# Performance work log

Hardware: AMD Instinct MI355X
Metric: run time of the kernel (lower is better)

## Reference

```python
import jax, jax.numpy as jnp
import numpy as np

AREA = 4
HEADS = 8

def conv1x1(x, W, b):
    # x: [B,C,H,W], W: [O,C], b: [O]
    return jnp.einsum('bchw,oc->bohw', x, W) + b[None, :, None, None]

def dwconv5(x, W, b):
    # depthwise 5x5, pad 2, groups = C; W: [C,1,5,5]
    C = x.shape[1]
    y = jax.lax.conv_general_dilated(
        x, W, window_strides=(1, 1), padding=[(2, 2), (2, 2)],
        dimension_numbers=('NCHW', 'OIHW', 'NCHW'), feature_group_count=C)
    return y + b[None, :, None, None]

def setup_inputs() -> dict:
    key = jax.random.key(0)
    ks = jax.random.split(key, 9)
    B, C, H, W = 4, 256, 64, 64
    s = 0.05
    return {
        'x': jax.random.normal(ks[0], (B, C, H, W), jnp.float32),
        'Wqk': jax.random.normal(ks[1], (2 * C, C), jnp.float32) * s,
        'bqk': jax.random.normal(ks[2], (2 * C,), jnp.float32) * s,
        'Wv': jax.random.normal(ks[3], (C, C), jnp.float32) * s,
        'bv': jax.random.normal(ks[4], (C,), jnp.float32) * s,
        'Wpe': jax.random.normal(ks[5], (C, 1, 5, 5), jnp.float32) * s,
        'bpe': jax.random.normal(ks[6], (C,), jnp.float32) * s,
        'Wproj': jax.random.normal(ks[7], (C, C), jnp.float32) * s,
        'bproj': jax.random.normal(ks[8], (C,), jnp.float32) * s,
    }

def reference(x, Wqk, bqk, Wv, bv, Wpe, bpe, Wproj, bproj):
    B, C, H, W = x.shape
    N = H * W
    hd = C // HEADS
    # qk / v projections (1x1 conv + folded BN bias, no activation)
    qk = conv1x1(x, Wqk, bqk).reshape(B, 2 * C, N).transpose(0, 2, 1)  # [B,N,2C]
    v4 = conv1x1(x, Wv, bv)                                            # [B,C,H,W]
    pp = dwconv5(v4, Wpe, bpe)                                         # positional enc
    v = v4.reshape(B, C, N).transpose(0, 2, 1)                         # [B,N,C]
    # area split: [B*area, N/area, .]
    Ba, Na = B * AREA, N // AREA
    qk = qk.reshape(Ba, Na, 2 * C)
    v = v.reshape(Ba, Na, C)
    q, k = qk[..., :C], qk[..., C:]
    q = q.reshape(Ba, Na, HEADS, hd)
    k = k.reshape(Ba, Na, HEADS, hd)
    v = v.reshape(Ba, Na, HEADS, hd)
    # manual softmax attention: (q^T k) * d^-0.5 -> softmax -> weight v
    attn = jnp.einsum('bqhd,bkhd->bhqk', q, k) * (hd ** -0.5)
    attn = jax.nn.softmax(attn, axis=-1)
    out = jnp.einsum('bhqk,bkhd->bqhd', attn, v)                       # [Ba,Na,H,hd]
    # merge areas back and go to NCHW
    out = out.reshape(B, N, C).reshape(B, H, W, C).transpose(0, 3, 1, 2)
    return conv1x1(out + pp, Wproj, bproj)
```

## Files before the change

kernel.cpp:

```cpp
#include <hip/hip_runtime.h>

typedef unsigned short u16;
typedef unsigned int u32;
using f32x4  = __attribute__((ext_vector_type(4))) float;
using u32x2  = __attribute__((ext_vector_type(2))) u32;
using u32x4  = __attribute__((ext_vector_type(4))) u32;
using bf16x8 = __attribute__((ext_vector_type(8))) short;

__device__ __forceinline__ u16 f2b(float f) {
  union { float f; u32 u; } v; v.f = f;
  return (u16)((v.u + 0x7FFFu + ((v.u >> 16) & 1u)) >> 16);
}
__device__ __forceinline__ float b2f(u16 u) {
  union { u32 u; float f; } v; v.u = ((u32)u) << 16;
  return v.f;
}
__device__ __forceinline__ u32 pk2(float a, float b) {
  u32 r;
  asm("v_cvt_pk_bf16_f32 %0, %1, %2" : "=v"(r) : "v"(a), "v"(b));
  return r;
}

__global__ __launch_bounds__(256) void kconvert(
    const float* __restrict__ Wqk, const float* __restrict__ Wv,
    const float* __restrict__ Wproj, u16* __restrict__ dst) {
  int e = (blockIdx.x * 256 + threadIdx.x) * 4;
  f32x4 v;
  if (e < 131072)      v = *(const f32x4*)(Wqk + e);
  else if (e < 196608) v = *(const f32x4*)(Wv + (e - 131072));
  else                 v = *(const f32x4*)(Wproj + (e - 196608));
  u32* d = (u32*)(dst + e);
  d[0] = (u32)f2b(v[0]) | ((u32)f2b(v[1]) << 16);
  d[1] = (u32)f2b(v[2]) | ((u32)f2b(v[3]) << 16);
}

__global__ __launch_bounds__(512) void kqkv(
    const float* __restrict__ x,
    const u16* __restrict__ Wqk_bf, const float* __restrict__ bqk,
    const u16* __restrict__ Wv_bf,  const float* __restrict__ bv,
    u16* __restrict__ qk_tm, u16* __restrict__ v_cm) {
  __shared__ __align__(16) u16 xs[64 * 264];
  const int bid = blockIdx.x;
  const int b   = bid >> 6;
  const int n0  = (bid & 63) * 64;
  const int tid = threadIdx.x;

  {
    const int part = tid & 15, cr = tid >> 4;
    #pragma unroll
    for (int p = 0; p < 8; ++p) {
      const int c = p * 32 + cr;
      f32x4 v = *(const f32x4*)(x + (size_t)(b * 256 + c) * 4096 + n0 + part * 4);
      const int t0 = part * 4;
      xs[(t0 + 0) * 264 + c] = f2b(v[0]);
      xs[(t0 + 1) * 264 + c] = f2b(v[1]);
      xs[(t0 + 2) * 264 + c] = f2b(v[2]);
      xs[(t0 + 3) * 264 + c] = f2b(v[3]);
    }
  }
  __syncthreads();

  const int wave = tid >> 6, l = tid & 63, lg = l & 15, lq = l >> 4;

  for (int ot = wave; ot < 48; ot += 8) {
    if (ot < 32) {
      bf16x8 bfr[8];
      const u16* wrow = Wqk_bf + (ot * 16 + lg) * 256 + lq * 8;
      #pragma unroll
      for (int kk = 0; kk < 8; ++kk) bfr[kk] = *(const bf16x8*)(wrow + kk * 32);
      const float bias = bqk[ot * 16 + lg];
      #pragma unroll
      for (int ts = 0; ts < 4; ++ts) {
        f32x4 acc = {0.f, 0.f, 0.f, 0.f};
        #pragma unroll
        for (int kk = 0; kk < 8; ++kk) {
          bf16x8 af = *(const bf16x8*)(&xs[(ts * 16 + lg) * 264 + kk * 32 + lq * 8]);
          acc = __builtin_amdgcn_mfma_f32_16x16x32_bf16(af, bfr[kk], acc, 0, 0, 0);
        }
        u16* dst = qk_tm + (size_t)(b * 4096 + n0 + ts * 16 + lq * 4) * 512 + ot * 16 + lg;
        #pragma unroll
        for (int r = 0; r < 4; ++r) dst[(size_t)r * 512] = f2b(acc[r] + bias);
      }
    } else {
      const int o2 = ot - 32;
      bf16x8 afw[8];
      const u16* wrow = Wv_bf + (o2 * 16 + lg) * 256 + lq * 8;
      #pragma unroll
      for (int kk = 0; kk < 8; ++kk) afw[kk] = *(const bf16x8*)(wrow + kk * 32);
      float bvr[4];
      #pragma unroll
      for (int r = 0; r < 4; ++r) bvr[r] = bv[o2 * 16 + lq * 4 + r];
      #pragma unroll
      for (int ts = 0; ts < 4; ++ts) {
        f32x4 acc = {0.f, 0.f, 0.f, 0.f};
        #pragma unroll
        for (int kk = 0; kk < 8; ++kk) {
          bf16x8 bfx = *(const bf16x8*)(&xs[(ts * 16 + lg) * 264 + kk * 32 + lq * 8]);
          acc = __builtin_amdgcn_mfma_f32_16x16x32_bf16(afw[kk], bfx, acc, 0, 0, 0);
        }
        #pragma unroll
        for (int r = 0; r < 4; ++r) {
          const int o = o2 * 16 + lq * 4 + r;
          v_cm[(size_t)(b * 256 + o) * 4096 + n0 + ts * 16 + lg] = f2b(acc[r] + bvr[r]);
        }
      }
    }
  }
}

__global__ __launch_bounds__(256) void kdw(
    const u16* __restrict__ v_cm, const float* __restrict__ Wpe,
    const float* __restrict__ bpe, u16* __restrict__ pp) {
  __shared__ __align__(16) u16 vsh[5 * 64 * 64];
  __shared__ float wsh[64 * 25];
  const int bid = blockIdx.x;
  const int ct = bid & 3, h = (bid >> 2) & 63, b = bid >> 8;
  const int c0 = ct * 64;
  const int tid = threadIdx.x;

  for (int i = tid; i < 64 * 25; i += 256) wsh[i] = Wpe[(c0 + i / 25) * 25 + i % 25];
  #pragma unroll
  for (int uu = 0; uu < 10; ++uu) {
    const int u = uu * 256 + tid;
    const int dy = u >> 9, rem = u & 511, c = rem >> 3, part = rem & 7;
    const int hy = h + dy - 2;
    u32x4 val = {0, 0, 0, 0};
    if (hy >= 0 && hy < 64)
      val = *(const u32x4*)(v_cm + (size_t)(b * 256 + c0 + c) * 4096 + hy * 64 + part * 8);
    *(u32x4*)(&vsh[(dy * 64 + c) * 64 + part * 8]) = val;
  }
  __syncthreads();

  const int c = tid >> 2, w0 = (tid & 3) * 16;
  float acc16[16];
  const float bias = bpe[c0 + c];
  #pragma unroll
  for (int i = 0; i < 16; ++i) acc16[i] = bias;
  const float* wc = &wsh[c * 25];
  #pragma unroll
  for (int dy = 0; dy < 5; ++dy) {
    const u16* row = &vsh[(dy * 64 + c) * 64];
    float rowv[20];
    #pragma unroll
    for (int j = 0; j < 20; ++j) {
      const int ww = w0 + j - 2;
      rowv[j] = (ww >= 0 && ww < 64) ? b2f(row[ww]) : 0.f;
    }
    #pragma unroll
    for (int dx = 0; dx < 5; ++dx) {
      const float wv = wc[dy * 5 + dx];
      #pragma unroll
      for (int wi = 0; wi < 16; ++wi) acc16[wi] += rowv[wi + dx] * wv;
    }
  }
  u32x4 o0, o1;
  #pragma unroll
  for (int i = 0; i < 4; ++i)
    o0[i] = (u32)f2b(acc16[2 * i]) | ((u32)f2b(acc16[2 * i + 1]) << 16);
  #pragma unroll
  for (int i = 0; i < 4; ++i)
    o1[i] = (u32)f2b(acc16[8 + 2 * i]) | ((u32)f2b(acc16[9 + 2 * i]) << 16);
  u16* dst = pp + (size_t)(b * 256 + c0 + c) * 4096 + h * 64 + w0;
  *(u32x4*)(dst) = o0;
  *(u32x4*)(dst + 8) = o1;
}

__global__ __launch_bounds__(256) void kattn(
    const u16* __restrict__ qk_tm, const u16* __restrict__ v_cm,
    u16* __restrict__ out_tm) {
  __shared__ __align__(16) char pbuf[4][32 * 128];

  const int bid = blockIdx.x;
  const int xcd = bid & 7, idx = bid >> 3;
  const int pair = xcd * 16 + (idx >> 3);
  const int qb = idx & 7;
  const int h = pair & 7, ba = pair >> 3;
  const int b = ba >> 2, area = ba & 3;
  const size_t row_base = (size_t)b * 4096 + area * 1024;

  const int tid = threadIdx.x;
  const int wave = tid >> 6, l = tid & 63, lg = l & 15, lq = l >> 4;
  char* pbc = pbuf[wave];
  const int swz = (lg & 7) << 4;
  const float kscale = 0.25503484f;

  bf16x8 bQ[2];
  #pragma unroll
  for (int s = 0; s < 2; ++s) {
    const size_t qrow = row_base + qb * 128 + wave * 32 + s * 16 + lg;
    bQ[s] = *(const bf16x8*)(qk_tm + qrow * 512 + h * 32 + lq * 8);
  }

  const u16* Kbase = qk_tm + row_base * 512 + 256 + h * 32 + lq * 8;
  const u16* Vbase = v_cm + (size_t)(b * 256 + h * 32) * 4096 + area * 1024 + lq * 8;

  f32x4 accO[2][2];
  float dAcc[2] = {0.f, 0.f};
  #pragma unroll
  for (int s = 0; s < 2; ++s)
    #pragma unroll
    for (int d = 0; d < 2; ++d) accO[s][d] = (f32x4){0.f, 0.f, 0.f, 0.f};

  bf16x8 fK0[4], fV0[4], fK1[4], fV1[4];

  auto LOAD = [&](bf16x8* fK, bf16x8* fV, int kb) {
    #pragma unroll
    for (int t = 0; t < 4; ++t)
      fK[t] = *(const bf16x8*)(Kbase + (size_t)(kb * 64 + t * 16 + lg) * 512);
    #pragma unroll
    for (int kk = 0; kk < 2; ++kk)
      #pragma unroll
      for (int dt = 0; dt < 2; ++dt)
        fV[kk * 2 + dt] = *(const bf16x8*)(Vbase + (size_t)(dt * 16 + lg) * 4096 + kb * 64 + kk * 32);
  };

  auto COMP = [&](bf16x8* fK, bf16x8* fV) {
    f32x4 sc[2][4];
    #pragma unroll
    for (int s = 0; s < 2; ++s)
      #pragma unroll
      for (int t = 0; t < 4; ++t) {
        f32x4 z = {0.f, 0.f, 0.f, 0.f};
        sc[s][t] = __builtin_amdgcn_mfma_f32_16x16x32_bf16(fK[t], bQ[s], z, 0, 0, 0);
      }
    #pragma unroll
    for (int s = 0; s < 2; ++s)
      #pragma unroll
      for (int t = 0; t < 4; ++t) {
        const float e0 = __builtin_amdgcn_exp2f(sc[s][t][0] * kscale);
        const float e1 = __builtin_amdgcn_exp2f(sc[s][t][1] * kscale);
        const float e2 = __builtin_amdgcn_exp2f(sc[s][t][2] * kscale);
        const float e3 = __builtin_amdgcn_exp2f(sc[s][t][3] * kscale);
        dAcc[s] += (e0 + e1) + (e2 + e3);
        u32x2 w = {pk2(e0, e1), pk2(e2, e3)};
        *(u32x2*)(pbc + (s * 16 + lg) * 128 + ((t * 32 + lq * 8) ^ swz)) = w;
      }
    asm volatile("s_waitcnt lgkmcnt(0)" ::: "memory");
    __builtin_amdgcn_sched_barrier(0);
    #pragma unroll
    for (int s = 0; s < 2; ++s)
      #pragma unroll
      for (int kk = 0; kk < 2; ++kk) {
        bf16x8 aP = *(const bf16x8*)(pbc + (s * 16 + lg) * 128 + ((kk * 64 + lq * 16) ^ swz));
        #pragma unroll
        for (int dt = 0; dt < 2; ++dt)
          accO[s][dt] = __builtin_amdgcn_mfma_f32_16x16x32_bf16(aP, fV[kk * 2 + dt], accO[s][dt], 0, 0, 0);
      }
  };

  LOAD(fK0, fV0, 0);
  for (int kb = 0; kb < 16; kb += 2) {
    LOAD(fK1, fV1, kb + 1);
    COMP(fK0, fV0);
    if (kb + 2 < 16) LOAD(fK0, fV0, kb + 2);
    COMP(fK1, fV1);
  }

  #pragma unroll
  for (int s = 0; s < 2; ++s) {
    float d = dAcc[s];
    d += __shfl_xor(d, 16);
    d += __shfl_xor(d, 32);
    #pragma unroll
    for (int r = 0; r < 4; ++r) {
      const float den = __shfl(d, lq * 4 + r);
      const float inv = __builtin_amdgcn_rcpf(den);
      const size_t row = row_base + qb * 128 + wave * 32 + s * 16 + lq * 4 + r;
      u16* dst = out_tm + row * 256 + h * 32 + lg;
      dst[0]  = f2b(accO[s][0][r] * inv);
      dst[16] = f2b(accO[s][1][r] * inv);
    }
  }
}

__global__ __launch_bounds__(512) void kproj(
    const u16* __restrict__ out_tm, const u16* __restrict__ pp,
    const u16* __restrict__ Wproj_bf, const float* __restrict__ bproj,
    float* __restrict__ out) {
  __shared__ __align__(16) u16 as_[64 * 264];
  const int bid = blockIdx.x;
  const int b = bid >> 6;
  const int n0 = (bid & 63) * 64;
  const int tid = threadIdx.x;
  {
    const int r = tid >> 3, qp = tid & 7;
    const u32x4* src = (const u32x4*)(out_tm + (size_t)(b * 4096 + n0 + r) * 256 + qp * 32);
    #pragma unroll
    for (int j = 0; j < 4; ++j)
      *(u32x4*)(&as_[r * 264 + qp * 32 + j * 8]) = src[j];
  }
  __syncthreads();
  {
    const int part = tid & 7;
    #pragma unroll
    for (int pass = 0; pass < 4; ++pass) {
      const int c = pass * 64 + (tid >> 3);
      u32x4 v = *(const u32x4*)(pp + (size_t)(b * 256 + c) * 4096 + n0 + part * 8);
      #pragma unroll
      for (int jj = 0; jj < 4; ++jj) {
        u32 w = v[jj];
        u16* q0 = &as_[(part * 8 + jj * 2) * 264 + c];
        *q0 = f2b(b2f(*q0) + b2f((u16)(w & 0xffffu)));
        u16* q1 = &as_[(part * 8 + jj * 2 + 1) * 264 + c];
        *q1 = f2b(b2f(*q1) + b2f((u16)(w >> 16)));
      }
    }
  }
  __syncthreads();
  const int wave = tid >> 6, l = tid & 63, lg = l & 15, lq = l >> 4;
  #pragma unroll
  for (int oi = 0; oi < 2; ++oi) {
    const int ot = oi * 8 + wave;
    bf16x8 afw[8];
    const u16* wrow = Wproj_bf + (ot * 16 + lg) * 256 + lq * 8;
    #pragma unroll
    for (int kk = 0; kk < 8; ++kk) afw[kk] = *(const bf16x8*)(wrow + kk * 32);
    float bpr[4];
    #pragma unroll
    for (int r = 0; r < 4; ++r) bpr[r] = bproj[ot * 16 + lq * 4 + r];
    #pragma unroll
    for (int ts = 0; ts < 4; ++ts) {
      f32x4 acc = {0.f, 0.f, 0.f, 0.f};
      #pragma unroll
      for (int kk = 0; kk < 8; ++kk) {
        bf16x8 bfx = *(const bf16x8*)(&as_[(ts * 16 + lg) * 264 + kk * 32 + lq * 8]);
        acc = __builtin_amdgcn_mfma_f32_16x16x32_bf16(afw[kk], bfx, acc, 0, 0, 0);
      }
      #pragma unroll
      for (int r = 0; r < 4; ++r) {
        const int o = ot * 16 + lq * 4 + r;
        out[(size_t)(b * 256 + o) * 4096 + n0 + ts * 16 + lg] = acc[r] + bpr[r];
      }
    }
  }
}

extern "C" void kernel_launch(void* const* d_in, const int* in_sizes, int n_in,
                              void* d_out, int out_size, void* d_ws, size_t ws_size,
                              hipStream_t stream) {
  const float* x     = (const float*)d_in[0];
  const float* Wqk   = (const float*)d_in[1];
  const float* bqk   = (const float*)d_in[2];
  const float* Wv    = (const float*)d_in[3];
  const float* bv    = (const float*)d_in[4];
  const float* Wpe   = (const float*)d_in[5];
  const float* bpe   = (const float*)d_in[6];
  const float* Wproj = (const float*)d_in[7];
  const float* bproj = (const float*)d_in[8];
  float* out = (float*)d_out;

  char* ws = (char*)d_ws;
  u16* qk_tm  = (u16*)(ws);
  u16* v_cm   = (u16*)(ws + 16777216);
  u16* pp     = (u16*)(ws + 25165824);
  u16* out_tm = (u16*)(ws + 33554432);
  u16* wbf    = (u16*)(ws + 41943040);
  u16* Wqk_bf = wbf;
  u16* Wv_bf = wbf + 131072;
  u16* Wproj_bf = wbf + 196608;

  kconvert<<<256, 256, 0, stream>>>(Wqk, Wv, Wproj, wbf);
  kqkv<<<256, 512, 0, stream>>>(x, Wqk_bf, bqk, Wv_bf, bv, qk_tm, v_cm);
  kdw<<<1024, 256, 0, stream>>>(v_cm, Wpe, bpe, pp);
  kattn<<<1024, 256, 0, stream>>>(qk_tm, v_cm, out_tm);
  kproj<<<256, 512, 0, stream>>>(out_tm, pp, Wproj_bf, bproj, out);
}
```

Measured before the change: 123.4 us.

## Split attention key range across wave pairs and reduce partials in LDS

Each attention block now covers 64 query rows instead of 128. Pairs of waves split the 1024-key range in half, and each wave loops over 8 key blocks instead of 16. The second wave of each pair writes its partial output accumulators and row sums to LDS, and the first wave adds them before normalizing and storing. This doubles the grid to 2048 blocks and halves the serial loop length per wave, which adds parallelism and shortens the tail. The cost is reloading Q tiles across more blocks, two extra block barriers and an LDS round trip for the reduction. It is only correct without a running max because the softmax uses plain exp sums.

```diff
diff --git a/kernel.cpp b/kernel.cpp
--- a/kernel.cpp
+++ b/kernel.cpp
@@ -169,17 +169,19 @@
     const u16* __restrict__ qk_tm, const u16* __restrict__ v_cm,
     u16* __restrict__ out_tm) {
   __shared__ __align__(16) char pbuf[4][32 * 128];
+  __shared__ float dbuf[4][32];
 
   const int bid = blockIdx.x;
   const int xcd = bid & 7, idx = bid >> 3;
-  const int pair = xcd * 16 + (idx >> 3);
-  const int qb = idx & 7;
+  const int pair = xcd * 16 + (idx >> 4);
+  const int qb = idx & 15;
   const int h = pair & 7, ba = pair >> 3;
   const int b = ba >> 2, area = ba & 3;
   const size_t row_base = (size_t)b * 4096 + area * 1024;
 
   const int tid = threadIdx.x;
   const int wave = tid >> 6, l = tid & 63, lg = l & 15, lq = l >> 4;
+  const int qhalf = wave >> 1, khalf = wave & 1;
   char* pbc = pbuf[wave];
   const int swz = (lg & 7) << 4;
   const float kscale = 0.25503484f;
@@ -187,12 +189,12 @@
   bf16x8 bQ[2];
   #pragma unroll
   for (int s = 0; s < 2; ++s) {
-    const size_t qrow = row_base + qb * 128 + wave * 32 + s * 16 + lg;
+    const size_t qrow = row_base + qb * 64 + qhalf * 32 + s * 16 + lg;
     bQ[s] = *(const bf16x8*)(qk_tm + qrow * 512 + h * 32 + lq * 8);
   }
 
-  const u16* Kbase = qk_tm + row_base * 512 + 256 + h * 32 + lq * 8;
-  const u16* Vbase = v_cm + (size_t)(b * 256 + h * 32) * 4096 + area * 1024 + lq * 8;
+  const u16* Kbase = qk_tm + (row_base + khalf * 512) * 512 + 256 + h * 32 + lq * 8;
+  const u16* Vbase = v_cm + (size_t)(b * 256 + h * 32) * 4096 + area * 1024 + khalf * 512 + lq * 8;
 
   f32x4 accO[2][2];
   float dAcc[2] = {0.f, 0.f};
@@ -249,26 +251,59 @@
   };
 
   LOAD(fK0, fV0, 0);
-  for (int kb = 0; kb < 16; kb += 2) {
+  for (int kb = 0; kb < 8; kb += 2) {
     LOAD(fK1, fV1, kb + 1);
     COMP(fK0, fV0);
-    if (kb + 2 < 16) LOAD(fK0, fV0, kb + 2);
+    if (kb + 2 < 8) LOAD(fK0, fV0, kb + 2);
     COMP(fK1, fV1);
   }
 
+  float dred[2];
   #pragma unroll
   for (int s = 0; s < 2; ++s) {
     float d = dAcc[s];
     d += __shfl_xor(d, 16);
     d += __shfl_xor(d, 32);
-    #pragma unroll
-    for (int r = 0; r < 4; ++r) {
-      const float den = __shfl(d, lq * 4 + r);
-      const float inv = __builtin_amdgcn_rcpf(den);
-      const size_t row = row_base + qb * 128 + wave * 32 + s * 16 + lq * 4 + r;
-      u16* dst = out_tm + row * 256 + h * 32 + lg;
-      dst[0]  = f2b(accO[s][0][r] * inv);
-      dst[16] = f2b(accO[s][1][r] * inv);
+    dred[s] = d;
+  }
+
+  __syncthreads();
+  if (khalf == 1) {
+    float* cb = (float*)pbuf[wave];
+    #pragma unroll
+    for (int s = 0; s < 2; ++s)
+      #pragma unroll
+      for (int dt = 0; dt < 2; ++dt)
+        #pragma unroll
+        for (int r = 0; r < 4; ++r)
+          cb[((s * 2 + dt) * 4 + r) * 64 + lq * 16 + lg] = accO[s][dt][r];
+    if (lq == 0) {
+      dbuf[wave][lg]      = dred[0];
+      dbuf[wave][16 + lg] = dred[1];
+    }
+  }
+  __syncthreads();
+  if (khalf == 0) {
+    const float* cb = (const float*)pbuf[wave + 1];
+    #pragma unroll
+    for (int s = 0; s < 2; ++s)
+      #pragma unroll
+      for (int dt = 0; dt < 2; ++dt)
+        #pragma unroll
+        for (int r = 0; r < 4; ++r)
+          accO[s][dt][r] += cb[((s * 2 + dt) * 4 + r) * 64 + lq * 16 + lg];
+    #pragma unroll
+    for (int s = 0; s < 2; ++s) {
+      const float dfull = dred[s] + dbuf[wave + 1][s * 16 + lg];
+      #pragma unroll
+      for (int r = 0; r < 4; ++r) {
+        const float den = __shfl(dfull, lq * 4 + r);
+        const float inv = __builtin_amdgcn_rcpf(den);
+        const size_t row = row_base + qb * 64 + qhalf * 32 + s * 16 + lq * 4 + r;
+        u16* dst = out_tm + row * 256 + h * 32 + lg;
+        dst[0]  = f2b(accO[s][0][r] * inv);
+        dst[16] = f2b(accO[s][1][r] * inv);
+      }
     }
   }
 }
@@ -362,6 +397,6 @@
   kconvert<<<256, 256, 0, stream>>>(Wqk, Wv, Wproj, wbf);
   kqkv<<<256, 512, 0, stream>>>(x, Wqk_bf, bqk, Wv_bf, bv, qk_tm, v_cm);
   kdw<<<1024, 256, 0, stream>>>(v_cm, Wpe, bpe, pp);
-  kattn<<<1024, 256, 0, stream>>>(qk_tm, v_cm, out_tm);
+  kattn<<<2048, 256, 0, stream>>>(qk_tm, v_cm, out_tm);
   kproj<<<256, 512, 0, stream>>>(out_tm, pp, Wproj_bf, bproj, out);
 }
```

Result: no change. 123.7 us (+0.2%).
